# Kernel optimization log

Hardware: AMD Instinct MI355X
Metric: run time of the kernel (lower is better)

The kernel has to match this reference:

```python
import jax, jax.numpy as jnp
import numpy as np

B, NK, NQ = 16, 1024, 1024
D_IN, D_V, D_H = 3, 8, 128
NUGGET = 1e-3   # diagonal regularizer for the kriging covariance solve
EPS = 1e-12     # keeps sqrt differentiable at zero distance


def _mlp(x, w1, b1, w2, b2, w3, b3):
    # Linear -> ReLU -> Linear -> ReLU -> Linear (torch Linear: y = x @ W.T + b)
    h = jax.nn.relu(x @ w1.T + b1)
    h = jax.nn.relu(h @ w2.T + b2)
    return h @ w3.T + b3


def _cdist(a, b):
    # a: [B,N,D], b: [B,M,D] -> [B,N,M] Euclidean distances
    d2 = (jnp.sum(a * a, -1)[:, :, None]
          + jnp.sum(b * b, -1)[:, None, :]
          - 2.0 * jnp.einsum('bnd,bmd->bnm', a, b))
    return jnp.sqrt(jnp.maximum(d2, 0.0) + EPS)


def _linear_init(key, out_f, in_f):
    k1, k2 = jax.random.split(key)
    lim = 1.0 / np.sqrt(in_f)
    w = jax.random.uniform(k1, (out_f, in_f), jnp.float32, -lim, lim)
    b = jax.random.uniform(k2, (out_f,), jnp.float32, -lim, lim)
    return w, b


def setup_inputs() -> dict:
    key = jax.random.key(0)
    ks = jax.random.split(key, 10)
    KEY = jax.random.normal(ks[0], (B, NK, D_IN), jnp.float32)
    VALUE = jax.random.normal(ks[1], (B, NK, D_V), jnp.float32)
    QUERY = jax.random.normal(ks[2], (B, NQ, D_IN), jnp.float32)
    W1_w, W1_b = _linear_init(ks[3], D_H, D_IN)
    W2_w, W2_b = _linear_init(ks[4], D_H, D_H)
    W3_w, W3_b = _linear_init(ks[5], D_IN, D_H)
    Wv1_w, Wv1_b = _linear_init(ks[6], D_H, D_V)
    Wv2_w, Wv2_b = _linear_init(ks[7], D_H, D_H)
    Wv3_w, Wv3_b = _linear_init(ks[8], D_V, D_H)
    return dict(KEY=KEY, VALUE=VALUE, QUERY=QUERY,
                W1_w=W1_w, W1_b=W1_b, W2_w=W2_w, W2_b=W2_b, W3_w=W3_w, W3_b=W3_b,
                Wv1_w=Wv1_w, Wv1_b=Wv1_b, Wv2_w=Wv2_w, Wv2_b=Wv2_b, Wv3_w=Wv3_w, Wv3_b=Wv3_b)


def reference(KEY, VALUE, QUERY,
              W1_w, W1_b, W2_w, W2_b, W3_w, W3_b,
              Wv1_w, Wv1_b, Wv2_w, Wv2_b, Wv3_w, Wv3_b):
    # shared MLP on KEY and QUERY, separate MLP on VALUE
    Wk = _mlp(KEY, W1_w, W1_b, W2_w, W2_b, W3_w, W3_b)
    Wq = _mlp(QUERY, W1_w, W1_b, W2_w, W2_b, W3_w, W3_b)
    Wv = _mlp(VALUE, Wv1_w, Wv1_b, Wv2_w, Wv2_b, Wv3_w, Wv3_b)
    VALUE_scale = VALUE * Wv                  # einsum('bij,bij->bij')
    # kriging prediction with learned elementwise coordinate scalings
    Ks = KEY * Wk                             # [B,NK,D_IN]
    Qs = QUERY * Wq                           # [B,NQ,D_IN]
    C_kk = jnp.exp(-_cdist(Ks, Ks)) + NUGGET * jnp.eye(NK, dtype=KEY.dtype)  # [B,NK,NK]
    C_qk = jnp.exp(-_cdist(Qs, Ks))                                          # [B,NQ,NK]
    # kriging weights: solve C_kk @ lam = C_qk^T  -> lam [B,NK,NQ]
    lam = jnp.linalg.solve(C_kk, jnp.swapaxes(C_qk, 1, 2))
    # prediction: weighted sum of scaled values -> [B,NQ,D_V]
    return jnp.einsum('bkq,bkv->bqv', lam, VALUE_scale)
```

## Files before the change

### kernel.cpp

```cpp
#include <hip/hip_runtime.h>
#include <hip/hip_bf16.h>


__device__ __forceinline__ int row_of(int e) {
    int i = (int)((sqrtf(8.0f * (float)e + 1.0f) - 1.0f) * 0.5f);
    while ((i + 1) * (i + 2) / 2 <= e) i++;
    while (i * (i + 1) / 2 > e) i--;
    return i;
}

__global__ void k_transpose(const float* __restrict__ W2, const float* __restrict__ Wv2,
                            float* __restrict__ W2T, float* __restrict__ Wv2T) {
    int tid = blockIdx.x * 256 + threadIdx.x;
    int e = tid & 16383;
    int r = e >> 7, c = e & 127;
    if (tid < 16384) W2T[c * 128 + r] = W2[e];
    else             Wv2T[c * 128 + r] = Wv2[e];
}

template<int DI, int P>
__device__ __forceinline__ void mlp_body(const float* __restrict__ in,
                                         float* __restrict__ out, int base,
                                         const float* __restrict__ W1,
                                         const float* __restrict__ b1,
                                         const float* __restrict__ W2T,
                                         const float* __restrict__ b2,
                                         const float* __restrict__ W3,
                                         const float* __restrict__ b3) {
    __shared__ float xs[P][DI];
    __shared__ float h1[P][128];
    __shared__ float h2[P][129];
    int t = threadIdx.x;
    for (int i = t; i < P * DI; i += 128) xs[i / DI][i % DI] = in[base * DI + i];
    __syncthreads();
    float w1r[DI];
#pragma unroll
    for (int d = 0; d < DI; d++) w1r[d] = W1[t * DI + d];
    float b1t = b1[t], b2t = b2[t];
#pragma unroll
    for (int p = 0; p < P; p++) {
        float s = b1t;
#pragma unroll
        for (int d = 0; d < DI; d++) s += w1r[d] * xs[p][d];
        h1[p][t] = fmaxf(s, 0.0f);
    }
    __syncthreads();
    float acc[P];
#pragma unroll
    for (int p = 0; p < P; p++) acc[p] = b2t;
    for (int k = 0; k < 128; k++) {
        float w = W2T[k * 128 + t];
#pragma unroll
        for (int p = 0; p < P; p++) acc[p] += w * h1[p][k];
    }
#pragma unroll
    for (int p = 0; p < P; p++) h2[p][t] = fmaxf(acc[p], 0.0f);
    __syncthreads();
    if (t < P * DI) {
        int p = t / DI, d = t % DI;
        float s = b3[d];
        for (int k = 0; k < 128; k++) s += W3[d * 128 + k] * h2[p][k];
        int gi = base * DI + t;
        out[gi] = in[gi] * s;
    }
}

__global__ void k_mlp_kq(const float* __restrict__ KEY, float* __restrict__ Ks,
                         const float* __restrict__ QUERY, float* __restrict__ Qs,
                         const float* __restrict__ W1, const float* __restrict__ b1,
                         const float* __restrict__ W2T, const float* __restrict__ b2,
                         const float* __restrict__ W3, const float* __restrict__ b3) {
    if (blockIdx.x < 512)
        mlp_body<3, 32>(KEY, Ks, blockIdx.x * 32, W1, b1, W2T, b2, W3, b3);
    else
        mlp_body<3, 32>(QUERY, Qs, (blockIdx.x - 512) * 32, W1, b1, W2T, b2, W3, b3);
}

__global__ void k_mlp_v(const float* __restrict__ VALUE, float* __restrict__ Vs,
                        const float* __restrict__ W1, const float* __restrict__ b1,
                        const float* __restrict__ W2T, const float* __restrict__ b2,
                        const float* __restrict__ W3, const float* __restrict__ b3) {
    mlp_body<8, 16>(VALUE, Vs, blockIdx.x * 16, W1, b1, W2T, b2, W3, b3);
}

__global__ void k_buildC(const float* __restrict__ Ks, float* __restrict__ C) {
    long idx = (long)blockIdx.x * 256 + threadIdx.x;
    int b = (int)(idx >> 20);
    int rem = (int)(idx & 1048575);
    int i = rem >> 10, j = rem & 1023;
    const float* a = Ks + ((long)b * 1024 + i) * 3;
    const float* bb = Ks + ((long)b * 1024 + j) * 3;
    float d0 = a[0] - bb[0], d1 = a[1] - bb[1], d2 = a[2] - bb[2];
    float dist = sqrtf(d0 * d0 + d1 * d1 + d2 * d2 + 1e-12f);
    float v = __expf(-dist);
    if (i == j) v += 1e-3f;
    C[idx] = v;
}

__device__ void potf_body(float* __restrict__ C, float* __restrict__ V,
                          float* smem, int o, int last, int b) {
    int tid = threadIdx.x;
    float* A = C + (long)b * 1048576;
    float* Vp = V + (long)b * 8192;
    float (*T)[132]      = (float(*)[132])smem;
    float (*cv)[8]       = (float(*)[8])(smem + 16896);
    float (*cw)[8]       = (float(*)[8])(smem + 17920);
    float (*Pn)[8]       = (float(*)[8])(smem + 18944);
    float (*St)[32][132] = (float(*)[32][132])(smem + 19968);
    float (*Lc)[32][33]  = (float(*)[32][33])(smem + 19968);
    float* rsd           = smem + 28416;
    float (*Wb)[32][33]  = (float(*)[32][33])(smem + 28544);
    float (*zs)[9]       = (float(*)[9])(smem + 30656);

    bool active = (tid < 272);
    int ti = 0, tj = 0, hh = 0;
    if (active) { int e = tid >> 1; hh = tid & 1; ti = row_of(e); tj = e - ti * (ti + 1) / 2; }
    int r0 = ti * 8 + hh * 4, c0t = tj * 8;
    int lane = tid & 63;
    int sr = tid >> 2, slk = (tid & 3) * 8;

    if (o > 0) {
        const float* sp = A + (long)(o + sr) * 1024 + (o - 128) + slk;
        float4 v0 = *(const float4*)sp;
        float4 v1 = *(const float4*)(sp + 4);
        St[0][slk    ][sr] = v0.x; St[0][slk + 1][sr] = v0.y;
        St[0][slk + 2][sr] = v0.z; St[0][slk + 3][sr] = v0.w;
        St[0][slk + 4][sr] = v1.x; St[0][slk + 5][sr] = v1.y;
        St[0][slk + 6][sr] = v1.z; St[0][slk + 7][sr] = v1.w;
    }
    float Treg[4][8];
    if (active) {
        const float* src = A + (long)(o + r0) * 1024 + o + c0t;
#pragma unroll
        for (int i = 0; i < 4; i++) {
            float4 va = *(const float4*)(src + (long)i * 1024);
            float4 vb = *(const float4*)(src + (long)i * 1024 + 4);
            Treg[i][0] = va.x; Treg[i][1] = va.y; Treg[i][2] = va.z; Treg[i][3] = va.w;
            Treg[i][4] = vb.x; Treg[i][5] = vb.y; Treg[i][6] = vb.z; Treg[i][7] = vb.w;
        }
    }
    if (o > 0) {
        for (int kc = 0; kc < 4; kc++) {
            __syncthreads();
            if (kc < 3) {
                const float* sp = A + (long)(o + sr) * 1024 + (o - 128) + (kc + 1) * 32 + slk;
                float4 v0 = *(const float4*)sp;
                float4 v1 = *(const float4*)(sp + 4);
                int nb = (kc + 1) & 1;
                St[nb][slk    ][sr] = v0.x; St[nb][slk + 1][sr] = v0.y;
                St[nb][slk + 2][sr] = v0.z; St[nb][slk + 3][sr] = v0.w;
                St[nb][slk + 4][sr] = v1.x; St[nb][slk + 5][sr] = v1.y;
                St[nb][slk + 6][sr] = v1.z; St[nb][slk + 7][sr] = v1.w;
            }
            if (active) {
                int buf = kc & 1;
#pragma unroll 4
                for (int k = 0; k < 32; k++) {
                    float4 a0 = *(const float4*)&St[buf][k][r0];
                    float4 b0 = *(const float4*)&St[buf][k][c0t];
                    float4 b1 = *(const float4*)&St[buf][k][c0t + 4];
                    float aa[4] = {a0.x, a0.y, a0.z, a0.w};
                    float bb[8] = {b0.x, b0.y, b0.z, b0.w, b1.x, b1.y, b1.z, b1.w};
#pragma unroll
                    for (int i = 0; i < 4; i++)
#pragma unroll
                        for (int j = 0; j < 8; j++) Treg[i][j] -= aa[i] * bb[j];
                }
            }
        }
    }
    if (active && tj == 0) {
#pragma unroll
        for (int i = 0; i < 4; i++) {
            *(float4*)&Pn[r0 + i][0] = make_float4(Treg[i][0], Treg[i][1], Treg[i][2], Treg[i][3]);
            *(float4*)&Pn[r0 + i][4] = make_float4(Treg[i][4], Treg[i][5], Treg[i][6], Treg[i][7]);
        }
    }
    __syncthreads();
    for (int jbt = 0; jbt < 16; jbt++) {
        int jb = jbt * 8;
        if (tid < 64) {
            int r1 = lane, r2 = 64 + lane;
            float v1[8], v2[8], w1[8], w2[8];
#pragma unroll
            for (int q = 0; q < 8; q++) {
                int j = jb + q;
                int jl = j & 63;
                bool hi = (j >= 64);
                float a1 = Pn[r1][q], a2 = Pn[r2][q];
#pragma unroll
                for (int p = 0; p < 8; p++) {
                    if (p < q) {
                        float wj = __shfl(hi ? w2[p] : w1[p], jl);
                        a1 -= v1[p] * wj;
                        a2 -= v2[p] * wj;
                    }
                }
                v1[q] = a1; v2[q] = a2;
                float dj = __shfl(hi ? a2 : a1, jl);
                float dinv = 1.0f / dj;
                w1[q] = a1 * dinv; w2[q] = a2 * dinv;
            }
            *(float4*)&cv[r1][0] = make_float4(v1[0], v1[1], v1[2], v1[3]);
            *(float4*)&cv[r1][4] = make_float4(v1[4], v1[5], v1[6], v1[7]);
            *(float4*)&cv[r2][0] = make_float4(v2[0], v2[1], v2[2], v2[3]);
            *(float4*)&cv[r2][4] = make_float4(v2[4], v2[5], v2[6], v2[7]);
            *(float4*)&cw[r1][0] = make_float4(w1[0], w1[1], w1[2], w1[3]);
            *(float4*)&cw[r1][4] = make_float4(w1[4], w1[5], w1[6], w1[7]);
            *(float4*)&cw[r2][0] = make_float4(w2[0], w2[1], w2[2], w2[3]);
            *(float4*)&cw[r2][4] = make_float4(w2[4], w2[5], w2[6], w2[7]);
        }
        __syncthreads();
        if (active && tj == jbt) {
#pragma unroll
            for (int i = 0; i < 4; i++) {
                float4 va = *(const float4*)&cv[r0 + i][0];
                float4 vb = *(const float4*)&cv[r0 + i][4];
                Treg[i][0] = va.x; Treg[i][1] = va.y; Treg[i][2] = va.z; Treg[i][3] = va.w;
                Treg[i][4] = vb.x; Treg[i][5] = vb.y; Treg[i][6] = vb.z; Treg[i][7] = vb.w;
            }
        } else if (active && tj > jbt) {
#pragma unroll
            for (int h = 0; h < 2; h++) {
                float va4[4][4], wb4[8][4];
#pragma unroll
                for (int i = 0; i < 4; i++) {
                    float4 v = *(const float4*)&cv[r0 + i][h * 4];
                    va4[i][0] = v.x; va4[i][1] = v.y; va4[i][2] = v.z; va4[i][3] = v.w;
                }
#pragma unroll
                for (int j = 0; j < 8; j++) {
                    float4 v = *(const float4*)&cw[c0t + j][h * 4];
                    wb4[j][0] = v.x; wb4[j][1] = v.y; wb4[j][2] = v.z; wb4[j][3] = v.w;
                }
#pragma unroll
                for (int i = 0; i < 4; i++)
#pragma unroll
                    for (int j = 0; j < 8; j++)
                        Treg[i][j] -= va4[i][0] * wb4[j][0] + va4[i][1] * wb4[j][1]
                                    + va4[i][2] * wb4[j][2] + va4[i][3] * wb4[j][3];
            }
            if (tj == jbt + 1) {
#pragma unroll
                for (int i = 0; i < 4; i++) {
                    *(float4*)&Pn[r0 + i][0] = make_float4(Treg[i][0], Treg[i][1], Treg[i][2], Treg[i][3]);
                    *(float4*)&Pn[r0 + i][4] = make_float4(Treg[i][4], Treg[i][5], Treg[i][6], Treg[i][7]);
                }
            }
        }
        __syncthreads();
    }
    if (active) {
#pragma unroll
        for (int i = 0; i < 4; i++) {
            *(float4*)&T[r0 + i][c0t]     = make_float4(Treg[i][0], Treg[i][1], Treg[i][2], Treg[i][3]);
            *(float4*)&T[r0 + i][c0t + 4] = make_float4(Treg[i][4], Treg[i][5], Treg[i][6], Treg[i][7]);
        }
    }
    __syncthreads();
    if (tid < 128) rsd[tid] = rsqrtf(T[tid][tid]);
    __syncthreads();
    {
        int rg = tid >> 5, cg = tid & 31;
#pragma unroll
        for (int j = 0; j < 4; j++) {
            int c = cg + 32 * j;
#pragma unroll
            for (int i = 0; i < 8; i++) {
                int r = rg * 8 + i;
                if (c <= r) T[r][c] *= rsd[c];
                else        T[r][c] = 0.0f;
            }
        }
    }
    __syncthreads();
    {
        int wv = tid >> 6;
        if (wv < 4 && lane < 32) {
            int d0 = wv * 32;
            int j = lane;
            float x[32];
#pragma unroll
            for (int i = 0; i < 32; i++) {
                float dinv = 1.0f / T[d0 + i][d0 + i];
                float s = 0.0f;
#pragma unroll
                for (int k = 0; k < i; k++) s += T[d0 + i][d0 + k] * x[k];
                x[i] = (i == j) ? dinv : -s * dinv;
            }
#pragma unroll
            for (int i = 0; i < 32; i++) T[d0 + i][d0 + j] = x[i];
        }
        if (tid >= 256) {
            for (int idx = tid - 256; idx < 6144; idx += 256) {
                int p = idx >> 10;
                int e = idx & 1023;
                int r = e >> 5, c = e & 31;
                int i3 = (p == 0) ? 1 : (p <= 2 ? 2 : 3);
                int kb = (p == 0) ? 0 : (p <= 2 ? p - 1 : p - 3);
                Lc[p][r][c] = T[i3 * 32 + r][kb * 32 + c];
            }
        }
    }
    __syncthreads();
    {
        int team = tid >> 8, ttid = tid & 255;
        int orr = ttid >> 3, oc = (ttid & 7) * 4;
        for (int st = 0; st < 3; st++) {
            int i3, j3;
            if (team == 0) { i3 = st + 1; j3 = 0; }
            else           { i3 = (st == 0) ? 2 : 3; j3 = (st == 2) ? 2 : 1; }
            float w0 = 0, w1 = 0, w2 = 0, w3 = 0;
            for (int kb = j3; kb < i3; kb++) {
                int p = i3 * (i3 - 1) / 2 + kb;
#pragma unroll 8
                for (int kk = 0; kk < 32; kk++) {
                    float l = Lc[p][orr][kk];
                    w0 += l * T[kb * 32 + kk][j3 * 32 + oc    ];
                    w1 += l * T[kb * 32 + kk][j3 * 32 + oc + 1];
                    w2 += l * T[kb * 32 + kk][j3 * 32 + oc + 2];
                    w3 += l * T[kb * 32 + kk][j3 * 32 + oc + 3];
                }
            }
            Wb[team][orr][oc] = w0; Wb[team][orr][oc + 1] = w1;
            Wb[team][orr][oc + 2] = w2; Wb[team][orr][oc + 3] = w3;
            __syncthreads();
            float v0 = 0, v1 = 0, v2 = 0, v3 = 0;
#pragma unroll 8
            for (int kk = 0; kk < 32; kk++) {
                float l = T[i3 * 32 + orr][i3 * 32 + kk];
                v0 += l * Wb[team][kk][oc    ];
                v1 += l * Wb[team][kk][oc + 1];
                v2 += l * Wb[team][kk][oc + 2];
                v3 += l * Wb[team][kk][oc + 3];
            }
            __syncthreads();
            T[i3 * 32 + orr][j3 * 32 + oc    ] = -v0;
            T[i3 * 32 + orr][j3 * 32 + oc + 1] = -v1;
            T[i3 * 32 + orr][j3 * 32 + oc + 2] = -v2;
            T[i3 * 32 + orr][j3 * 32 + oc + 3] = -v3;
            __syncthreads();
        }
    }
    {
        int r = tid >> 2, c0 = (tid & 3) * 32;
        float* dst = A + (long)(o + r) * 1024 + o + c0;
#pragma unroll
        for (int k = 0; k < 8; k++) {
            int c = c0 + 4 * k;
            *(float4*)(dst + 4 * k) = make_float4(T[r][c], T[r][c + 1], T[r][c + 2], T[r][c + 3]);
        }
    }
    {
        int k = tid >> 2, c2 = (tid & 3) * 2;
        float2 v = *(const float2*)&Vp[(o + k) * 8 + c2];
        zs[k][c2] = v.x; zs[k][c2 + 1] = v.y;
    }
    __syncthreads();
    {
        int r = tid & 127, c2 = (tid >> 7) * 2;
        float y0 = 0, y1 = 0;
#pragma unroll 8
        for (int k = 0; k < 128; k++) {
            float l = T[r][k];
            y0 += l * zs[k][c2];
            y1 += l * zs[k][c2 + 1];
        }
        if (!last) {
            *(float2*)&Vp[(o + r) * 8 + c2] = make_float2(y0, y1);
        } else {
            __syncthreads();
            zs[r][c2] = y0; zs[r][c2 + 1] = y1;
            __syncthreads();
            float x0 = 0, x1 = 0;
#pragma unroll 8
            for (int k = 0; k < 128; k++) {
                float l = T[k][r];
                x0 += l * zs[k][c2];
                x1 += l * zs[k][c2 + 1];
            }
            *(float2*)&Vp[(o + r) * 8 + c2] = make_float2(x0, x1);
        }
    }
}

__device__ void syrk_body(float* __restrict__ C, float* smem,
                          int o, int pti, int ptj, int b) {
    float* A = C + (long)b * 1048576;
    int bi = o + 128 + pti * 128, bj = o + 128 + ptj * 128;
    float (*As)[132] = (float(*)[132])smem;
    float (*Bs)[132] = (float(*)[132])(smem + 4224);
    int tid = threadIdx.x;
    int tx = tid & 15, ty = tid >> 4;
    float acc[4][8] = {};
    int lr = tid >> 2;
    int lk = (tid & 3) * 8;
    bool diag = (bi == bj);
    for (int kc = 0; kc < 128; kc += 32) {
        {
            const float* src = A + (long)(bi + lr) * 1024 + o + kc + lk;
            float4 v0 = *(const float4*)src;
            float4 v1 = *(const float4*)(src + 4);
            As[lk    ][lr] = v0.x; As[lk + 1][lr] = v0.y;
            As[lk + 2][lr] = v0.z; As[lk + 3][lr] = v0.w;
            As[lk + 4][lr] = v1.x; As[lk + 5][lr] = v1.y;
            As[lk + 6][lr] = v1.z; As[lk + 7][lr] = v1.w;
            if (!diag) {
                const float* sb = A + (long)(bj + lr) * 1024 + o + kc + lk;
                float4 w0 = *(const float4*)sb;
                float4 w1 = *(const float4*)(sb + 4);
                Bs[lk    ][lr] = w0.x; Bs[lk + 1][lr] = w0.y;
                Bs[lk + 2][lr] = w0.z; Bs[lk + 3][lr] = w0.w;
                Bs[lk + 4][lr] = w1.x; Bs[lk + 5][lr] = w1.y;
                Bs[lk + 6][lr] = w1.z; Bs[lk + 7][lr] = w1.w;
            }
        }
        __syncthreads();
        {
            float (*Bp)[132] = diag ? As : Bs;
#pragma unroll
            for (int k = 0; k < 32; k++) {
                float4 a0 = *(const float4*)&As[k][ty * 4];
                float4 b0 = *(const float4*)&Bp[k][tx * 8];
                float4 b1 = *(const float4*)&Bp[k][tx * 8 + 4];
                float aa[4] = {a0.x, a0.y, a0.z, a0.w};
                float bb[8] = {b0.x, b0.y, b0.z, b0.w, b1.x, b1.y, b1.z, b1.w};
#pragma unroll
                for (int i = 0; i < 4; i++)
#pragma unroll
                    for (int j = 0; j < 8; j++) acc[i][j] += aa[i] * bb[j];
            }
        }
        __syncthreads();
    }
#pragma unroll
    for (int i = 0; i < 4; i++) {
        int r = bi + ty * 4 + i;
        float* dst = A + (long)r * 1024 + bj + tx * 8;
        if (!diag) {
            float4 p0 = *(const float4*)dst;
            float4 p1 = *(const float4*)(dst + 4);
            p0.x -= acc[i][0]; p0.y -= acc[i][1]; p0.z -= acc[i][2]; p0.w -= acc[i][3];
            p1.x -= acc[i][4]; p1.y -= acc[i][5]; p1.z -= acc[i][6]; p1.w -= acc[i][7];
            *(float4*)dst = p0;
            *(float4*)(dst + 4) = p1;
        } else {
#pragma unroll
            for (int j = 0; j < 8; j++) {
                int c = bj + tx * 8 + j;
                if (c <= r) dst[j] -= acc[i][j];
            }
        }
    }
}

__global__ __launch_bounds__(512) void k_potf_syrk(float* __restrict__ C,
                                                   float* __restrict__ V,
                                                   int o, int last) {
    __shared__ __align__(16) float smem[31808];
    int bx = blockIdx.x;
    if (bx < 16) {
        potf_body(C, V, smem, o, last, bx);
    } else {
        int v = bx - 16;
        int bb = v & 15;
        int p = (v >> 4) + 1;
        int tii = row_of(p);
        int tjj = p - tii * (tii + 1) / 2;
        syrk_body(C, smem, o - 128, tii, tjj, bb);
    }
}

__global__ __launch_bounds__(256) void k_trsmg(float* __restrict__ C,
                                               float* __restrict__ V, int o) {
    int b = blockIdx.y;
    float* A = C + (long)b * 1048576;
    float* Vp = V + (long)b * 8192;
    int bi = o + 128 + blockIdx.x * 128;
    const float* Linv = A + (long)o * 1024 + o;
    __shared__ float As[32][132];
    __shared__ float Ls[32][132];
    int tid = threadIdx.x;
    int tx = tid & 15, ty = tid >> 4;
    float acc[8][8] = {};
    int lr = tid >> 1;
    int lk = (tid & 1) * 16;
    for (int kc = 0; kc < 128; kc += 32) {
        const float* src = A + (long)(bi + lr) * 1024 + o + kc + lk;
        const float* sl  = Linv + (long)lr * 1024 + kc + lk;
#pragma unroll
        for (int k4 = 0; k4 < 4; k4++) {
            float4 v = *(const float4*)(src + 4 * k4);
            As[lk + 4*k4    ][lr] = v.x;
            As[lk + 4*k4 + 1][lr] = v.y;
            As[lk + 4*k4 + 2][lr] = v.z;
            As[lk + 4*k4 + 3][lr] = v.w;
            float4 w = *(const float4*)(sl + 4 * k4);
            Ls[lk + 4*k4    ][lr] = w.x;
            Ls[lk + 4*k4 + 1][lr] = w.y;
            Ls[lk + 4*k4 + 2][lr] = w.z;
            Ls[lk + 4*k4 + 3][lr] = w.w;
        }
        __syncthreads();
#pragma unroll
        for (int k = 0; k < 32; k++) {
            float4 a0 = *(const float4*)&As[k][ty * 8];
            float4 a1 = *(const float4*)&As[k][ty * 8 + 4];
            float4 b0 = *(const float4*)&Ls[k][tx * 8];
            float4 b1 = *(const float4*)&Ls[k][tx * 8 + 4];
            float aa[8] = {a0.x,a0.y,a0.z,a0.w,a1.x,a1.y,a1.z,a1.w};
            float bb[8] = {b0.x,b0.y,b0.z,b0.w,b1.x,b1.y,b1.z,b1.w};
#pragma unroll
            for (int i = 0; i < 8; i++)
#pragma unroll
                for (int j = 0; j < 8; j++) acc[i][j] += aa[i] * bb[j];
        }
        __syncthreads();
    }
#pragma unroll
    for (int i = 0; i < 8; i++) {
        float* dst = A + (long)(bi + ty * 8 + i) * 1024 + o + tx * 8;
        *(float4*)dst       = make_float4(acc[i][0], acc[i][1], acc[i][2], acc[i][3]);
        *(float4*)(dst + 4) = make_float4(acc[i][4], acc[i][5], acc[i][6], acc[i][7]);
    }
    float* ysf = &Ls[0][0];
    {
        int k = tid >> 1, c0 = (tid & 1) * 4;
        float4 v = *(const float4*)&Vp[(o + k) * 8 + c0];
        ysf[k * 9 + c0] = v.x; ysf[k * 9 + c0 + 1] = v.y;
        ysf[k * 9 + c0 + 2] = v.z; ysf[k * 9 + c0 + 3] = v.w;
    }
    __syncthreads();
    float zacc0 = 0, zacc1 = 0, zacc2 = 0, zacc3 = 0;
    int zr = tid & 127, zc0 = (tid >> 7) * 4;
#pragma unroll
    for (int ch = 0; ch < 4; ch++) {
        if ((tx >> 2) == ch) {
            int cb = (tx & 3) * 8;
#pragma unroll
            for (int j = 0; j < 8; j++)
#pragma unroll
                for (int i = 0; i < 8; i++)
                    As[cb + j][ty * 8 + i] = acc[i][j];
        }
        __syncthreads();
#pragma unroll 8
        for (int k = 0; k < 32; k++) {
            float l = As[k][zr];
            const float* yp = &ysf[(ch * 32 + k) * 9 + zc0];
            zacc0 += l * yp[0]; zacc1 += l * yp[1];
            zacc2 += l * yp[2]; zacc3 += l * yp[3];
        }
        __syncthreads();
    }
    float* vp = &Vp[(bi + zr) * 8 + zc0];
    float4 old = *(const float4*)vp;
    old.x -= zacc0; old.y -= zacc1; old.z -= zacc2; old.w -= zacc3;
    *(float4*)vp = old;
}

__global__ __launch_bounds__(256) void k_bstep(const float* __restrict__ C,
                                               float* __restrict__ V, int k) {
    int b = blockIdx.y, j = blockIdx.x, tid = threadIdx.x;
    const float* A = C + (long)b * 1048576;
    float* Vp = V + (long)b * 8192;
    __shared__ float Lb[128][129];
    __shared__ float xs[128][9];
    __shared__ float ys[128][9];
    {
        int kk = tid >> 1, c0 = (tid & 1) * 4;
        float4 v = *(const float4*)&Vp[(k * 128 + kk) * 8 + c0];
        xs[kk][c0] = v.x; xs[kk][c0+1] = v.y; xs[kk][c0+2] = v.z; xs[kk][c0+3] = v.w;
    }
#pragma unroll
    for (int m = 0; m < 16; m++) {
        int e = tid + m * 256;
        int i = e >> 5, j4 = (e & 31) * 4;
        float4 v = *(const float4*)&A[(long)(k * 128 + i) * 1024 + j * 128 + j4];
        Lb[i][j4] = v.x; Lb[i][j4+1] = v.y; Lb[i][j4+2] = v.z; Lb[i][j4+3] = v.w;
    }
    __syncthreads();
    int r = tid & 127, c0 = (tid >> 7) * 4;
    float u0 = 0, u1 = 0, u2 = 0, u3 = 0;
#pragma unroll 8
    for (int kk = 0; kk < 128; kk++) {
        float l = Lb[kk][r];
        u0 += l * xs[kk][c0    ];
        u1 += l * xs[kk][c0 + 1];
        u2 += l * xs[kk][c0 + 2];
        u3 += l * xs[kk][c0 + 3];
    }
    float* vp = &Vp[(j * 128 + r) * 8 + c0];
    float4 old = *(const float4*)vp;
    old.x -= u0; old.y -= u1; old.z -= u2; old.w -= u3;
    if (j < k - 1) {
        *(float4*)vp = old;
    } else {
        ys[r][c0] = old.x; ys[r][c0+1] = old.y; ys[r][c0+2] = old.z; ys[r][c0+3] = old.w;
        __syncthreads();
        int o = j * 128;
#pragma unroll
        for (int m = 0; m < 16; m++) {
            int e = tid + m * 256;
            int i = e >> 5, j4 = (e & 31) * 4;
            float4 v = *(const float4*)&A[(long)(o + i) * 1024 + o + j4];
            Lb[i][j4] = v.x; Lb[i][j4+1] = v.y; Lb[i][j4+2] = v.z; Lb[i][j4+3] = v.w;
        }
        __syncthreads();
        float x0 = 0, x1 = 0, x2 = 0, x3 = 0;
#pragma unroll 8
        for (int kk = 0; kk < 128; kk++) {
            float l = Lb[kk][r];
            x0 += l * ys[kk][c0    ];
            x1 += l * ys[kk][c0 + 1];
            x2 += l * ys[kk][c0 + 2];
            x3 += l * ys[kk][c0 + 3];
        }
        *(float4*)vp = make_float4(x0, x1, x2, x3);
    }
}

__global__ void k_out(const float* __restrict__ Qs, const float* __restrict__ Ks,
                      const float* __restrict__ X, float* __restrict__ out) {
    int b = blockIdx.x >> 4;
    int qc = blockIdx.x & 15;
    int t = threadIdx.x;
    int q = t & 63, ks = t >> 6;
    __shared__ float kx[1024][3];
    __shared__ __align__(16) float xv[1024][8];
    __shared__ float red[4][64][8];
    for (int i = t; i < 3072; i += 256) kx[i / 3][i % 3] = Ks[b * 3072 + i];
    for (int i = t; i < 8192; i += 256) xv[i >> 3][i & 7] = X[b * 8192 + i];
    __syncthreads();
    int gq = b * 1024 + qc * 64 + q;
    const float* qp = Qs + (long)gq * 3;
    float qx = qp[0], qy = qp[1], qz = qp[2];
    float acc[8] = {};
    int k0 = ks * 256;
#pragma unroll 2
    for (int k = k0; k < k0 + 256; k++) {
        float dx = qx - kx[k][0], dy = qy - kx[k][1], dz = qz - kx[k][2];
        float w = __expf(-sqrtf(dx * dx + dy * dy + dz * dz + 1e-12f));
        float4 xa = *(const float4*)&xv[k][0];
        float4 xb = *(const float4*)&xv[k][4];
        acc[0] += w * xa.x; acc[1] += w * xa.y; acc[2] += w * xa.z; acc[3] += w * xa.w;
        acc[4] += w * xb.x; acc[5] += w * xb.y; acc[6] += w * xb.z; acc[7] += w * xb.w;
    }
#pragma unroll
    for (int c = 0; c < 8; c++) red[ks][q][c] = acc[c];
    __syncthreads();
    if (ks == 0) {
        float* op = out + (long)gq * 8;
#pragma unroll
        for (int c = 0; c < 8; c++)
            op[c] = red[0][q][c] + red[1][q][c] + red[2][q][c] + red[3][q][c];
    }
}

extern "C" void kernel_launch(void* const* d_in, const int* in_sizes, int n_in,
                              void* d_out, int out_size, void* d_ws, size_t ws_size,
                              hipStream_t stream) {
    const float* KEY   = (const float*)d_in[0];
    const float* VALUE = (const float*)d_in[1];
    const float* QUERY = (const float*)d_in[2];
    const float* W1w = (const float*)d_in[3];  const float* W1b = (const float*)d_in[4];
    const float* W2w = (const float*)d_in[5];  const float* W2b = (const float*)d_in[6];
    const float* W3w = (const float*)d_in[7];  const float* W3b = (const float*)d_in[8];
    const float* Wv1w = (const float*)d_in[9]; const float* Wv1b = (const float*)d_in[10];
    const float* Wv2w = (const float*)d_in[11];const float* Wv2b = (const float*)d_in[12];
    const float* Wv3w = (const float*)d_in[13];const float* Wv3b = (const float*)d_in[14];

    float* ws  = (float*)d_ws;
    float* C    = ws;
    float* Ks   = C + 16777216;
    float* Qs   = Ks + 49152;
    float* Vs   = Qs + 49152;
    float* W2T  = Vs + 131072;
    float* Wv2T = W2T + 16384;

    float* out = (float*)d_out;

    hipLaunchKernelGGL(k_transpose, dim3(128), dim3(256), 0, stream, W2w, Wv2w, W2T, Wv2T);
    hipLaunchKernelGGL(k_mlp_kq, dim3(1024), dim3(128), 0, stream,
                       KEY, Ks, QUERY, Qs, W1w, W1b, W2T, W2b, W3w, W3b);
    hipLaunchKernelGGL(k_mlp_v, dim3(1024), dim3(128), 0, stream,
                       VALUE, Vs, Wv1w, Wv1b, Wv2T, Wv2b, Wv3w, Wv3b);
    hipLaunchKernelGGL(k_buildC, dim3(65536), dim3(256), 0, stream, Ks, C);

    for (int s = 0; s < 8; s++) {
        int o = s * 128;
        int np = 0;
        if (s >= 1) { int ntp = 8 - s; np = ntp * (ntp + 1) / 2 - 1; }
        hipLaunchKernelGGL(k_potf_syrk, dim3(16 + np * 16), dim3(512), 0, stream,
                           C, Vs, o, (s == 7) ? 1 : 0);
        int nt = 7 - s;
        if (nt > 0)
            hipLaunchKernelGGL(k_trsmg, dim3(nt, 16), dim3(256), 0, stream, C, Vs, o);
    }
    for (int k = 7; k >= 1; k--)
        hipLaunchKernelGGL(k_bstep, dim3(k, 16), dim3(256), 0, stream, C, Vs, k);

    hipLaunchKernelGGL(k_out, dim3(256), dim3(256), 0, stream, Qs, Ks, Vs, out);
}
```

Before: 998.5 us.

## Pipeline panel LDL with trailing update and widen trsm blocks to 512 threads

In the per-batch 128x128 diagonal block factorization, the 8-column panel factorization (ldl8) for the next block column now runs on a spare wavefront in double-buffered shared memory while the other threads do the trailing update. The block column that feeds the next panel is updated first, which shortens the serial critical path. One __syncthreads in the inner-block solve is removed. k_trsmg goes from 256 to 512 threads with half the accumulator tile per thread, for more parallelism per block at the cost of extra shared-memory traffic and a larger shared-memory footprint in potf.

```diff
diff --git a/kernel.cpp b/kernel.cpp
--- a/kernel.cpp
+++ b/kernel.cpp
@@ -97,20 +97,79 @@
     C[idx] = v;
 }
 
+__device__ __forceinline__ void panel_update(float Treg[4][8], const float (*cv)[8],
+                                             const float (*cw)[8], int r0, int c0t) {
+#pragma unroll
+    for (int h = 0; h < 2; h++) {
+        float va4[4][4], wb4[8][4];
+#pragma unroll
+        for (int i = 0; i < 4; i++) {
+            float4 v = *(const float4*)&cv[r0 + i][h * 4];
+            va4[i][0] = v.x; va4[i][1] = v.y; va4[i][2] = v.z; va4[i][3] = v.w;
+        }
+#pragma unroll
+        for (int j = 0; j < 8; j++) {
+            float4 v = *(const float4*)&cw[c0t + j][h * 4];
+            wb4[j][0] = v.x; wb4[j][1] = v.y; wb4[j][2] = v.z; wb4[j][3] = v.w;
+        }
+#pragma unroll
+        for (int i = 0; i < 4; i++)
+#pragma unroll
+            for (int j = 0; j < 8; j++)
+                Treg[i][j] -= va4[i][0] * wb4[j][0] + va4[i][1] * wb4[j][1]
+                            + va4[i][2] * wb4[j][2] + va4[i][3] * wb4[j][3];
+    }
+}
+
+__device__ __forceinline__ void ldl8(int lane, int jb, const float (*Pn)[8],
+                                     float (*cv)[8], float (*cw)[8]) {
+    int r1 = lane, r2 = 64 + lane;
+    float v1[8], v2[8], w1[8], w2[8];
+#pragma unroll
+    for (int q = 0; q < 8; q++) {
+        int j = jb + q;
+        int jl = j & 63;
+        bool hi = (j >= 64);
+        float a1 = Pn[r1][q], a2 = Pn[r2][q];
+#pragma unroll
+        for (int p = 0; p < 8; p++) {
+            if (p < q) {
+                float wj = __shfl(hi ? w2[p] : w1[p], jl);
+                a1 -= v1[p] * wj;
+                a2 -= v2[p] * wj;
+            }
+        }
+        v1[q] = a1; v2[q] = a2;
+        float dj = __shfl(hi ? a2 : a1, jl);
+        float dinv = 1.0f / dj;
+        w1[q] = a1 * dinv; w2[q] = a2 * dinv;
+    }
+    *(float4*)&cv[r1][0] = make_float4(v1[0], v1[1], v1[2], v1[3]);
+    *(float4*)&cv[r1][4] = make_float4(v1[4], v1[5], v1[6], v1[7]);
+    *(float4*)&cv[r2][0] = make_float4(v2[0], v2[1], v2[2], v2[3]);
+    *(float4*)&cv[r2][4] = make_float4(v2[4], v2[5], v2[6], v2[7]);
+    *(float4*)&cw[r1][0] = make_float4(w1[0], w1[1], w1[2], w1[3]);
+    *(float4*)&cw[r1][4] = make_float4(w1[4], w1[5], w1[6], w1[7]);
+    *(float4*)&cw[r2][0] = make_float4(w2[0], w2[1], w2[2], w2[3]);
+    *(float4*)&cw[r2][4] = make_float4(w2[4], w2[5], w2[6], w2[7]);
+}
+
 __device__ void potf_body(float* __restrict__ C, float* __restrict__ V,
                           float* smem, int o, int last, int b) {
     int tid = threadIdx.x;
     float* A = C + (long)b * 1048576;
     float* Vp = V + (long)b * 8192;
     float (*T)[132]      = (float(*)[132])smem;
-    float (*cv)[8]       = (float(*)[8])(smem + 16896);
-    float (*cw)[8]       = (float(*)[8])(smem + 17920);
+    float (*cv0)[8]      = (float(*)[8])(smem + 16896);
+    float (*cw0)[8]      = (float(*)[8])(smem + 17920);
     float (*Pn)[8]       = (float(*)[8])(smem + 18944);
     float (*St)[32][132] = (float(*)[32][132])(smem + 19968);
     float (*Lc)[32][33]  = (float(*)[32][33])(smem + 19968);
     float* rsd           = smem + 28416;
     float (*Wb)[32][33]  = (float(*)[32][33])(smem + 28544);
     float (*zs)[9]       = (float(*)[9])(smem + 30656);
+    float (*cv1)[8]      = (float(*)[8])(smem + 31808);
+    float (*cw1)[8]      = (float(*)[8])(smem + 32832);
 
     bool active = (tid < 272);
     int ti = 0, tj = 0, hh = 0;
@@ -177,78 +236,37 @@
         }
     }
     __syncthreads();
+    if (tid >= 448) ldl8(tid - 448, 0, Pn, cv0, cw0);
+    __syncthreads();
+    int cur = 0;
     for (int jbt = 0; jbt < 16; jbt++) {
-        int jb = jbt * 8;
-        if (tid < 64) {
-            int r1 = lane, r2 = 64 + lane;
-            float v1[8], v2[8], w1[8], w2[8];
-#pragma unroll
-            for (int q = 0; q < 8; q++) {
-                int j = jb + q;
-                int jl = j & 63;
-                bool hi = (j >= 64);
-                float a1 = Pn[r1][q], a2 = Pn[r2][q];
-#pragma unroll
-                for (int p = 0; p < 8; p++) {
-                    if (p < q) {
-                        float wj = __shfl(hi ? w2[p] : w1[p], jl);
-                        a1 -= v1[p] * wj;
-                        a2 -= v2[p] * wj;
-                    }
-                }
-                v1[q] = a1; v2[q] = a2;
-                float dj = __shfl(hi ? a2 : a1, jl);
-                float dinv = 1.0f / dj;
-                w1[q] = a1 * dinv; w2[q] = a2 * dinv;
-            }
-            *(float4*)&cv[r1][0] = make_float4(v1[0], v1[1], v1[2], v1[3]);
-            *(float4*)&cv[r1][4] = make_float4(v1[4], v1[5], v1[6], v1[7]);
-            *(float4*)&cv[r2][0] = make_float4(v2[0], v2[1], v2[2], v2[3]);
-            *(float4*)&cv[r2][4] = make_float4(v2[4], v2[5], v2[6], v2[7]);
-            *(float4*)&cw[r1][0] = make_float4(w1[0], w1[1], w1[2], w1[3]);
-            *(float4*)&cw[r1][4] = make_float4(w1[4], w1[5], w1[6], w1[7]);
-            *(float4*)&cw[r2][0] = make_float4(w2[0], w2[1], w2[2], w2[3]);
-            *(float4*)&cw[r2][4] = make_float4(w2[4], w2[5], w2[6], w2[7]);
-        }
-        __syncthreads();
+        float (*cvc)[8] = cur ? cv1 : cv0;
+        float (*cwc)[8] = cur ? cw1 : cw0;
         if (active && tj == jbt) {
 #pragma unroll
             for (int i = 0; i < 4; i++) {
-                float4 va = *(const float4*)&cv[r0 + i][0];
-                float4 vb = *(const float4*)&cv[r0 + i][4];
+                float4 va = *(const float4*)&cvc[r0 + i][0];
+                float4 vb = *(const float4*)&cvc[r0 + i][4];
                 Treg[i][0] = va.x; Treg[i][1] = va.y; Treg[i][2] = va.z; Treg[i][3] = va.w;
                 Treg[i][4] = vb.x; Treg[i][5] = vb.y; Treg[i][6] = vb.z; Treg[i][7] = vb.w;
             }
-        } else if (active && tj > jbt) {
-#pragma unroll
-            for (int h = 0; h < 2; h++) {
-                float va4[4][4], wb4[8][4];
-#pragma unroll
-                for (int i = 0; i < 4; i++) {
-                    float4 v = *(const float4*)&cv[r0 + i][h * 4];
-                    va4[i][0] = v.x; va4[i][1] = v.y; va4[i][2] = v.z; va4[i][3] = v.w;
-                }
-#pragma unroll
-                for (int j = 0; j < 8; j++) {
-                    float4 v = *(const float4*)&cw[c0t + j][h * 4];
-                    wb4[j][0] = v.x; wb4[j][1] = v.y; wb4[j][2] = v.z; wb4[j][3] = v.w;
-                }
-#pragma unroll
-                for (int i = 0; i < 4; i++)
-#pragma unroll
-                    for (int j = 0; j < 8; j++)
-                        Treg[i][j] -= va4[i][0] * wb4[j][0] + va4[i][1] * wb4[j][1]
-                                    + va4[i][2] * wb4[j][2] + va4[i][3] * wb4[j][3];
-            }
-            if (tj == jbt + 1) {
-#pragma unroll
-                for (int i = 0; i < 4; i++) {
-                    *(float4*)&Pn[r0 + i][0] = make_float4(Treg[i][0], Treg[i][1], Treg[i][2], Treg[i][3]);
-                    *(float4*)&Pn[r0 + i][4] = make_float4(Treg[i][4], Treg[i][5], Treg[i][6], Treg[i][7]);
-                }
-            }
-        }
-        __syncthreads();
+        } else if (active && tj == jbt + 1) {
+            panel_update(Treg, cvc, cwc, r0, c0t);
+#pragma unroll
+            for (int i = 0; i < 4; i++) {
+                *(float4*)&Pn[r0 + i][0] = make_float4(Treg[i][0], Treg[i][1], Treg[i][2], Treg[i][3]);
+                *(float4*)&Pn[r0 + i][4] = make_float4(Treg[i][4], Treg[i][5], Treg[i][6], Treg[i][7]);
+            }
+        }
+        __syncthreads();
+        if (tid >= 448) {
+            if (jbt < 15)
+                ldl8(tid - 448, (jbt + 1) * 8, Pn, cur ? cv0 : cv1, cur ? cw0 : cw1);
+        } else if (active && tj > jbt + 1) {
+            panel_update(Treg, cvc, cwc, r0, c0t);
+        }
+        __syncthreads();
+        cur ^= 1;
     }
     if (active) {
 #pragma unroll
@@ -334,7 +352,6 @@
                 v2 += l * Wb[team][kk][oc + 2];
                 v3 += l * Wb[team][kk][oc + 3];
             }
-            __syncthreads();
             T[i3 * 32 + orr][j3 * 32 + oc    ] = -v0;
             T[i3 * 32 + orr][j3 * 32 + oc + 1] = -v1;
             T[i3 * 32 + orr][j3 * 32 + oc + 2] = -v2;
@@ -457,7 +474,7 @@
 __global__ __launch_bounds__(512) void k_potf_syrk(float* __restrict__ C,
                                                    float* __restrict__ V,
                                                    int o, int last) {
-    __shared__ __align__(16) float smem[31808];
+    __shared__ __align__(16) float smem[33856];
     int bx = blockIdx.x;
     if (bx < 16) {
         potf_body(C, V, smem, o, last, bx);
@@ -471,7 +488,7 @@
     }
 }
 
-__global__ __launch_bounds__(256) void k_trsmg(float* __restrict__ C,
+__global__ __launch_bounds__(512) void k_trsmg(float* __restrict__ C,
                                                float* __restrict__ V, int o) {
     int b = blockIdx.y;
     float* A = C + (long)b * 1048576;
@@ -482,57 +499,56 @@
     __shared__ float Ls[32][132];
     int tid = threadIdx.x;
     int tx = tid & 15, ty = tid >> 4;
-    float acc[8][8] = {};
-    int lr = tid >> 1;
-    int lk = (tid & 1) * 16;
+    float acc[4][8] = {};
+    int lr = tid >> 2;
+    int lk = (tid & 3) * 8;
     for (int kc = 0; kc < 128; kc += 32) {
-        const float* src = A + (long)(bi + lr) * 1024 + o + kc + lk;
-        const float* sl  = Linv + (long)lr * 1024 + kc + lk;
-#pragma unroll
-        for (int k4 = 0; k4 < 4; k4++) {
-            float4 v = *(const float4*)(src + 4 * k4);
-            As[lk + 4*k4    ][lr] = v.x;
-            As[lk + 4*k4 + 1][lr] = v.y;
-            As[lk + 4*k4 + 2][lr] = v.z;
-            As[lk + 4*k4 + 3][lr] = v.w;
-            float4 w = *(const float4*)(sl + 4 * k4);
-            Ls[lk + 4*k4    ][lr] = w.x;
-            Ls[lk + 4*k4 + 1][lr] = w.y;
-            Ls[lk + 4*k4 + 2][lr] = w.z;
-            Ls[lk + 4*k4 + 3][lr] = w.w;
+        {
+            const float* src = A + (long)(bi + lr) * 1024 + o + kc + lk;
+            const float* sl  = Linv + (long)lr * 1024 + kc + lk;
+            float4 v0 = *(const float4*)src;
+            float4 v1 = *(const float4*)(src + 4);
+            As[lk    ][lr] = v0.x; As[lk + 1][lr] = v0.y;
+            As[lk + 2][lr] = v0.z; As[lk + 3][lr] = v0.w;
+            As[lk + 4][lr] = v1.x; As[lk + 5][lr] = v1.y;
+            As[lk + 6][lr] = v1.z; As[lk + 7][lr] = v1.w;
+            float4 w0 = *(const float4*)sl;
+            float4 w1 = *(const float4*)(sl + 4);
+            Ls[lk    ][lr] = w0.x; Ls[lk + 1][lr] = w0.y;
+            Ls[lk + 2][lr] = w0.z; Ls[lk + 3][lr] = w0.w;
+            Ls[lk + 4][lr] = w1.x; Ls[lk + 5][lr] = w1.y;
+            Ls[lk + 6][lr] = w1.z; Ls[lk + 7][lr] = w1.w;
         }
         __syncthreads();
 #pragma unroll
         for (int k = 0; k < 32; k++) {
-            float4 a0 = *(const float4*)&As[k][ty * 8];
-            float4 a1 = *(const float4*)&As[k][ty * 8 + 4];
+            float4 a0 = *(const float4*)&As[k][ty * 4];
             float4 b0 = *(const float4*)&Ls[k][tx * 8];
             float4 b1 = *(const float4*)&Ls[k][tx * 8 + 4];
-            float aa[8] = {a0.x,a0.y,a0.z,a0.w,a1.x,a1.y,a1.z,a1.w};
-            float bb[8] = {b0.x,b0.y,b0.z,b0.w,b1.x,b1.y,b1.z,b1.w};
-#pragma unroll
-            for (int i = 0; i < 8; i++)
+            float aa[4] = {a0.x, a0.y, a0.z, a0.w};
+            float bb[8] = {b0.x, b0.y, b0.z, b0.w, b1.x, b1.y, b1.z, b1.w};
+#pragma unroll
+            for (int i = 0; i < 4; i++)
 #pragma unroll
                 for (int j = 0; j < 8; j++) acc[i][j] += aa[i] * bb[j];
         }
         __syncthreads();
     }
 #pragma unroll
-    for (int i = 0; i < 8; i++) {
-        float* dst = A + (long)(bi + ty * 8 + i) * 1024 + o + tx * 8;
+    for (int i = 0; i < 4; i++) {
+        float* dst = A + (long)(bi + ty * 4 + i) * 1024 + o + tx * 8;
         *(float4*)dst       = make_float4(acc[i][0], acc[i][1], acc[i][2], acc[i][3]);
         *(float4*)(dst + 4) = make_float4(acc[i][4], acc[i][5], acc[i][6], acc[i][7]);
     }
     float* ysf = &Ls[0][0];
     {
-        int k = tid >> 1, c0 = (tid & 1) * 4;
-        float4 v = *(const float4*)&Vp[(o + k) * 8 + c0];
-        ysf[k * 9 + c0] = v.x; ysf[k * 9 + c0 + 1] = v.y;
-        ysf[k * 9 + c0 + 2] = v.z; ysf[k * 9 + c0 + 3] = v.w;
-    }
-    __syncthreads();
-    float zacc0 = 0, zacc1 = 0, zacc2 = 0, zacc3 = 0;
-    int zr = tid & 127, zc0 = (tid >> 7) * 4;
+        int k = tid >> 2, c2 = (tid & 3) * 2;
+        float2 v = *(const float2*)&Vp[(o + k) * 8 + c2];
+        ysf[k * 9 + c2] = v.x; ysf[k * 9 + c2 + 1] = v.y;
+    }
+    __syncthreads();
+    float zacc0 = 0, zacc1 = 0;
+    int zr = tid & 127, zc0 = (tid >> 7) * 2;
 #pragma unroll
     for (int ch = 0; ch < 4; ch++) {
         if ((tx >> 2) == ch) {
@@ -540,8 +556,8 @@
 #pragma unroll
             for (int j = 0; j < 8; j++)
 #pragma unroll
-                for (int i = 0; i < 8; i++)
-                    As[cb + j][ty * 8 + i] = acc[i][j];
+                for (int i = 0; i < 4; i++)
+                    As[cb + j][ty * 4 + i] = acc[i][j];
         }
         __syncthreads();
 #pragma unroll 8
@@ -549,14 +565,13 @@
             float l = As[k][zr];
             const float* yp = &ysf[(ch * 32 + k) * 9 + zc0];
             zacc0 += l * yp[0]; zacc1 += l * yp[1];
-            zacc2 += l * yp[2]; zacc3 += l * yp[3];
         }
         __syncthreads();
     }
     float* vp = &Vp[(bi + zr) * 8 + zc0];
-    float4 old = *(const float4*)vp;
-    old.x -= zacc0; old.y -= zacc1; old.z -= zacc2; old.w -= zacc3;
-    *(float4*)vp = old;
+    float2 old = *(const float2*)vp;
+    old.x -= zacc0; old.y -= zacc1;
+    *(float2*)vp = old;
 }
 
 __global__ __launch_bounds__(256) void k_bstep(const float* __restrict__ C,
@@ -695,7 +710,7 @@
                            C, Vs, o, (s == 7) ? 1 : 0);
         int nt = 7 - s;
         if (nt > 0)
-            hipLaunchKernelGGL(k_trsmg, dim3(nt, 16), dim3(256), 0, stream, C, Vs, o);
+            hipLaunchKernelGGL(k_trsmg, dim3(nt, 16), dim3(512), 0, stream, C, Vs, o);
     }
     for (int k = 7; k >= 1; k--)
         hipLaunchKernelGGL(k_bstep, dim3(k, 16), dim3(256), 0, stream, C, Vs, k);
```

After: 1.071 ms. 1.07x slower.
